# Kernel optimization log

Measured on AMD Instinct MI355X. Metric: run time of the kernel, lower is better.

## Reference

```python
import jax, jax.numpy as jnp
import numpy as np

ALPHA = 0.2  # leaky relu slope
NEG = -9e15


def setup_inputs() -> dict:
    key = jax.random.key(0)
    k1, k2, k3, k4 = jax.random.split(key, 4)
    B, N, Fin, Fout = 16, 2048, 256, 256
    h = jax.random.normal(k1, (B, N, Fin), dtype=jnp.float32)
    adj = jax.random.randint(k2, (B, N, N), 0, 2, dtype=jnp.int32)
    # xavier_uniform with gain 1.414 on [B, Fin, Fout] (fan over last two dims)
    limW = 1.414 * np.sqrt(6.0 / (Fin + Fout))
    W = jax.random.uniform(k3, (B, Fin, Fout), minval=-limW, maxval=limW, dtype=jnp.float32)
    lima = 1.414 * np.sqrt(6.0 / (2 * Fout + 1))
    a = jax.random.uniform(k4, (B, 2 * Fout, 1), minval=-lima, maxval=lima, dtype=jnp.float32)
    return {"h": h, "adj": adj, "W": W, "a": a}


def reference(h, adj, W, a):
    Fout = W.shape[-1]
    Wh = jnp.einsum('bnf,bfo->bno', h, W)                 # [B,N,Fout]
    Wh1 = jnp.einsum('bno,bo->bn', Wh, a[:, :Fout, 0])    # [B,N]
    Wh2 = jnp.einsum('bno,bo->bn', Wh, a[:, Fout:, 0])    # [B,N]
    e = Wh1[:, :, None] + Wh2[:, None, :]                 # [B,N,N]
    e = jnp.where(e > 0, e, ALPHA * e)                    # leaky relu
    att = jnp.where(adj > 0, e, NEG)
    att = jax.nn.softmax(att, axis=1)                     # NOTE: dim=1 as in source
    # dropout: eval mode -> identity
    h_prime = jnp.einsum('bij,bjo->bio', att, Wh)         # [B,N,Fout]
    return jax.nn.elu(h_prime)                            # concat=True
```

## Files before the change

### kernel.cpp

```cpp
#include <hip/hip_runtime.h>
#include <hip/hip_bf16.h>

typedef unsigned short u16;
typedef unsigned long long u64;
typedef __attribute__((ext_vector_type(8))) short bf16x8;
typedef __attribute__((ext_vector_type(4))) float f32x4;

#define NB 16
#define NN 2048
#define FF 256
#define LOG2E 1.4426950408889634f

__device__ __forceinline__ u16 f2bf(float x) {
    union { float f; unsigned u; } v; v.f = x;
    unsigned r = v.u + 0x7fffu + ((v.u >> 16) & 1u);
    return (u16)(r >> 16);
}

#define GLD_LDS(g, l) __builtin_amdgcn_global_load_lds((const __attribute__((address_space(1))) void*)(g), (__attribute__((address_space(3))) void*)(l), 16, 0, 0)

__global__ __launch_bounds__(256) void k_prep_w(const float* __restrict__ W, const float* __restrict__ a,
                                                u16* __restrict__ WT, float* __restrict__ u1, float* __restrict__ u2) {
    int b = blockIdx.y, t = threadIdx.x;
    __shared__ float a1s[FF], a2s[FF];
    a1s[t] = a[b*2*FF + t];
    a2s[t] = a[b*2*FF + FF + t];
    __syncthreads();
    int f = blockIdx.x*64 + (t >> 2);
    int o0 = (t & 3) * 64;
    const float* wrow = W + (size_t)(b*FF + f)*FF + o0;
    u16* wtb = WT + (size_t)b*FF*FF;
    float s1 = 0.f, s2 = 0.f;
#pragma unroll
    for (int c = 0; c < 16; ++c) {
        float4 v = *(const float4*)(wrow + c*4);
        int o = o0 + c*4;
        s1 += v.x*a1s[o] + v.y*a1s[o+1] + v.z*a1s[o+2] + v.w*a1s[o+3];
        s2 += v.x*a2s[o] + v.y*a2s[o+1] + v.z*a2s[o+2] + v.w*a2s[o+3];
        wtb[(size_t)(o+0)*FF + f] = f2bf(v.x);
        wtb[(size_t)(o+1)*FF + f] = f2bf(v.y);
        wtb[(size_t)(o+2)*FF + f] = f2bf(v.z);
        wtb[(size_t)(o+3)*FF + f] = f2bf(v.w);
    }
    s1 += __shfl_xor(s1, 1); s1 += __shfl_xor(s1, 2);
    s2 += __shfl_xor(s2, 1); s2 += __shfl_xor(s2, 2);
    if ((t & 3) == 0) { u1[b*FF + f] = s1; u2[b*FF + f] = s2; }
}

__global__ __launch_bounds__(256) void k_wh(const float* __restrict__ h, const u16* __restrict__ WT,
                                            const float* __restrict__ u1, const float* __restrict__ u2,
                                            u16* __restrict__ WhT, float* __restrict__ Wh1, float* __restrict__ Wh2) {
    int bid = blockIdx.x;
    int nid = (bid & 7)*64 + (bid >> 3);
    int b  = nid >> 5;
    int i0 = (nid & 31) * 64;
    int t = threadIdx.x, lane = t & 63, wave = t >> 6;
    __shared__ alignas(16) u16 At[256*64];
    __shared__ alignas(16) u16 Bt[64*64];
    __shared__ float u1s[FF], u2s[FF];
    u1s[t] = u1[b*FF + t];
    u2s[t] = u2[b*FF + t];

    const u16*   WTb = WT + (size_t)b*FF*FF;
    const float* hb  = h + ((size_t)b*NN + i0)*FF;
    int r = t >> 2, q = t & 3, kq = q*16;

    f32x4 acc[4][4];
#pragma unroll
    for (int x = 0; x < 4; ++x)
#pragma unroll
        for (int y = 0; y < 4; ++y) acc[x][y] = (f32x4)0.f;
    float s1 = 0.f, s2 = 0.f;
    __syncthreads();

#pragma unroll 1
    for (int kk = 0; kk < 4; ++kk) {
        int k0 = kk*64;
#pragma unroll
        for (int is = 0; is < 8; ++is) {
            int s = is*256 + t;
            int row = s >> 3, jbp = s & 7;
            int jbl = jbp ^ (row & 7);
            GLD_LDS(WTb + (size_t)row*FF + k0 + jbl*8, &At[s*8]);
        }
        {
            const float* hp = hb + (size_t)r*FF + k0 + kq;
            float4 f0 = *(const float4*)(hp + 0);
            float4 f1 = *(const float4*)(hp + 4);
            float4 f2 = *(const float4*)(hp + 8);
            float4 f3 = *(const float4*)(hp + 12);
            float fv[16] = {f0.x,f0.y,f0.z,f0.w, f1.x,f1.y,f1.z,f1.w,
                            f2.x,f2.y,f2.z,f2.w, f3.x,f3.y,f3.z,f3.w};
            union { u16 u[16]; bf16x8 v[2]; } cv;
#pragma unroll
            for (int e = 0; e < 16; ++e) {
                int kidx = k0 + kq + e;
                s1 += fv[e]*u1s[kidx];
                s2 += fv[e]*u2s[kidx];
                cv.u[e] = f2bf(fv[e]);
            }
            int rx = r & 7;
            *(bf16x8*)&Bt[r*64 + ((q*2 + 0) ^ rx)*8] = cv.v[0];
            *(bf16x8*)&Bt[r*64 + ((q*2 + 1) ^ rx)*8] = cv.v[1];
        }
        __syncthreads();
#pragma unroll
        for (int kc = 0; kc < 2; ++kc) {
            int jl = kc*4 + (lane >> 4);
            bf16x8 af[4], bfr[4];
#pragma unroll
            for (int mi = 0; mi < 4; ++mi) {
                int rr2 = wave*64 + mi*16 + (lane & 15);
                af[mi] = *(const bf16x8*)&At[rr2*64 + ((jl ^ (rr2 & 7))*8)];
            }
#pragma unroll
            for (int ni = 0; ni < 4; ++ni) {
                int rr2 = ni*16 + (lane & 15);
                bfr[ni] = *(const bf16x8*)&Bt[rr2*64 + ((jl ^ (rr2 & 7))*8)];
            }
#pragma unroll
            for (int mi = 0; mi < 4; ++mi)
#pragma unroll
                for (int ni = 0; ni < 4; ++ni)
                    acc[mi][ni] = __builtin_amdgcn_mfma_f32_16x16x32_bf16(af[mi], bfr[ni], acc[mi][ni], 0, 0, 0);
        }
        __syncthreads();
    }
    s1 += __shfl_xor(s1, 1); s1 += __shfl_xor(s1, 2);
    s2 += __shfl_xor(s2, 1); s2 += __shfl_xor(s2, 2);
    if (q == 0) { Wh1[b*NN + i0 + r] = s1*LOG2E; Wh2[b*NN + i0 + r] = s2*LOG2E; }

    u16* Wo = WhT + (size_t)b*FF*NN;
#pragma unroll
    for (int mi = 0; mi < 4; ++mi)
#pragma unroll
        for (int ni = 0; ni < 4; ++ni) {
            int i = i0 + ni*16 + (lane & 15);
#pragma unroll
            for (int rr = 0; rr < 4; ++rr) {
                int o = wave*64 + mi*16 + (lane >> 4)*4 + rr;
                Wo[(size_t)o*NN + i] = f2bf(acc[mi][ni][rr]);
            }
        }
}

__global__ __launch_bounds__(256) void k_pack(const int* __restrict__ adj, const float* __restrict__ Wh1,
                                              const float* __restrict__ Wh2, float* __restrict__ pS,
                                              u64* __restrict__ packed) {
    int b = blockIdx.y, ic = blockIdx.x;
    int t = threadIdx.x;
    __shared__ float wh1s[64], e1ps[64], e1ns[64];
    __shared__ unsigned char mk[64][256];
    int ibase = ic*64;
    if (t < 64) {
        float w1 = Wh1[b*NN + ibase + t];
        wh1s[t] = w1;
        e1ps[t] = __builtin_amdgcn_exp2f(w1);
        e1ns[t] = __builtin_amdgcn_exp2f(0.2f*w1);
    }
    float w2[8];
    {
        float4 a0 = *(const float4*)(Wh2 + b*NN + t*8);
        float4 a1 = *(const float4*)(Wh2 + b*NN + t*8 + 4);
        w2[0]=a0.x; w2[1]=a0.y; w2[2]=a0.z; w2[3]=a0.w;
        w2[4]=a1.x; w2[5]=a1.y; w2[6]=a1.z; w2[7]=a1.w;
    }
    __syncthreads();
    const int* abase = adj + ((size_t)(b*NN + ibase))*NN + t*8;
    float sp[8] = {0.f,0.f,0.f,0.f,0.f,0.f,0.f,0.f};
    float sn[8] = {0.f,0.f,0.f,0.f,0.f,0.f,0.f,0.f};
#pragma unroll 1
    for (int r4 = 0; r4 < 16; ++r4) {
        int4 v[4][2];
#pragma unroll
        for (int k = 0; k < 4; ++k) {
            v[k][0] = *(const int4*)(abase + (size_t)(r4*4 + k)*NN);
            v[k][1] = *(const int4*)(abase + (size_t)(r4*4 + k)*NN + 4);
        }
#pragma unroll
        for (int k = 0; k < 4; ++k) {
            int row = r4*4 + k;
            float w1 = wh1s[row], ep = e1ps[row], en = e1ns[row];
            int a[8] = {v[k][0].x, v[k][0].y, v[k][0].z, v[k][0].w,
                        v[k][1].x, v[k][1].y, v[k][1].z, v[k][1].w};
            unsigned bits = 0;
#pragma unroll
            for (int e = 0; e < 8; ++e) {
                bool bit = a[e] > 0;
                bool pos = (w1 + w2[e]) > 0.f;
                bits |= bit ? (1u << e) : 0u;
                sp[e] += (bit && pos)  ? ep : 0.f;
                sn[e] += (bit && !pos) ? en : 0.f;
            }
            mk[row][t] = (unsigned char)bits;
        }
    }
    __syncthreads();
    {
        int g = t >> 3, r0 = (t & 7)*8;
        u64* dst = packed + ((size_t)(b*32 + g))*NN + ibase + r0;
#pragma unroll
        for (int k = 0; k < 8; ++k)
            dst[k] = *(const u64*)&mk[r0 + k][g*8];
    }
    {
        float o8[8];
#pragma unroll
        for (int e = 0; e < 8; ++e) {
            float E2p = __builtin_amdgcn_exp2f(w2[e]);
            float E2n = __builtin_amdgcn_exp2f(0.2f*w2[e]);
            o8[e] = E2p*sp[e] + E2n*sn[e];
        }
        float4* po = (float4*)(pS + ((size_t)(b*32 + ic))*NN + t*8);
        po[0] = make_float4(o8[0],o8[1],o8[2],o8[3]);
        po[1] = make_float4(o8[4],o8[5],o8[6],o8[7]);
    }
}

__global__ __launch_bounds__(512, 1) void k_gemm3(const u16* __restrict__ WhT, const u64* __restrict__ packed,
                                                  const float* __restrict__ Wh1, const float* __restrict__ Wh2,
                                                  const float* __restrict__ pS, float* __restrict__ out) {
    int bid = blockIdx.x;
    int nid = (bid & 7)*32 + (bid >> 3);
    int b  = nid >> 4;
    int i0 = (nid & 15) * 128;
    int t = threadIdx.x, lane = t & 63, wave = t >> 6;
    int wm = wave >> 2, wn = wave & 3;
    __shared__ alignas(16) u16 At[2][128*64];
    __shared__ alignas(16) u16 Bt[3][256*64];
    __shared__ float wh2s[NN];
    __shared__ float e2ps[NN];
    __shared__ float e2ns[NN];
    __shared__ unsigned zlut[4];

    const u16* Wo = WhT + (size_t)b*FF*NN;
    int rA = t >> 2, qA = t & 3;
    const u64* pkbase = packed + (size_t)b*32*NN + i0 + rA;

    float wh1r = Wh1[b*NN + i0 + rA];
    float e1p = __builtin_amdgcn_exp2f(wh1r);
    float e1n = __builtin_amdgcn_exp2f(0.2f*wh1r);

#pragma unroll
    for (int c = 0; c < 4; ++c) {
        int idx = c*512 + t;
        float w2 = Wh2[b*NN + idx];
        float s = 0.f;
#pragma unroll
        for (int cc = 0; cc < 32; ++cc) s += pS[((size_t)(b*32 + cc))*NN + idx];
        float inv = (s > 0.f) ? 1.0f/s : 0.0f;
        wh2s[idx] = w2;
        e2ps[idx] = __builtin_amdgcn_exp2f(w2) * inv;
        e2ns[idx] = __builtin_amdgcn_exp2f(0.2f*w2) * inv;
    }
    if (t < 4) zlut[t] = ((t & 1) ? 0xFFFFu : 0u) | ((t & 2) ? 0xFFFF0000u : 0u);

    auto stageB = [&](int kk, int bbuf) {
        int k0 = kk*64;
#pragma unroll
        for (int is = 0; is < 4; ++is) {
            int s = is*512 + t;
            int row = s >> 3, jbp = s & 7;
            int jbl = jbp ^ (row & 7);
            GLD_LDS(Wo + (size_t)row*NN + k0 + jbl*8, &Bt[bbuf][s*8]);
        }
    };
    auto genA = [&](int g, int abuf, unsigned mask16) {
        int rx = rA & 7;
#pragma unroll
        for (int hf = 0; hf < 2; ++hf) {
            union { unsigned w[4]; bf16x8 v; } ob;
#pragma unroll
            for (int q4 = 0; q4 < 2; ++q4) {
                int jb = g*64 + qA*16 + hf*8 + q4*4;
                float4 w2 = *(const float4*)&wh2s[jb];
                float4 tp = *(const float4*)&e2ps[jb];
                float4 tn = *(const float4*)&e2ns[jb];
                float xs[4] = {w2.x, w2.y, w2.z, w2.w};
                float ps[4] = {tp.x, tp.y, tp.z, tp.w};
                float ns[4] = {tn.x, tn.y, tn.z, tn.w};
                float pe[4];
#pragma unroll
                for (int e = 0; e < 4; ++e) {
                    float tt = wh1r + xs[e];
                    bool pos = tt > 0.f;
                    pe[e] = (pos ? e1p : e1n) * (pos ? ps[e] : ns[e]);
                }
                unsigned bits = mask16 >> (hf*8 + q4*4);
#pragma unroll
                for (int p = 0; p < 2; ++p) {
                    unsigned w;
                    asm("v_cvt_pk_bf16_f32 %0, %1, %2" : "=v"(w) : "v"(pe[2*p]), "v"(pe[2*p+1]));
                    ob.w[q4*2 + p] = w & zlut[(bits >> (2*p)) & 3];
                }
            }
            *(bf16x8*)&At[abuf][rA*64 + (((qA*2 + hf) ^ rx)*8)] = ob.v;
        }
    };

#define MM(mi, ni, af, bf) acc[mi][ni] = __builtin_amdgcn_mfma_f32_16x16x32_bf16(af, bf, acc[mi][ni], 0, 0, 0)

    f32x4 acc[4][4];
#pragma unroll
    for (int x = 0; x < 4; ++x)
#pragma unroll
        for (int y = 0; y < 4; ++y) acc[x][y] = (f32x4)0.f;

    u64 mcur = pkbase[0];
    u64 mnext = pkbase[NN];
    __syncthreads();
    stageB(0, 0);
    stageB(1, 1);
    genA(0, 0, (unsigned)((mcur >> (qA*16)) & 0xffffu));
    asm volatile("s_waitcnt vmcnt(4) lgkmcnt(0)" ::: "memory");
    __builtin_amdgcn_s_barrier();

    int ibr = 0, ibs = 2;
#pragma unroll 1
    for (int kk = 0; kk < 32; ++kk) {
        int g = kk + 1;
        bool havef = (kk + 2 < 32);
        u64 mfut = 0;
        if (havef) mfut = pkbase[(size_t)(kk + 2)*NN];
        if (havef) stageB(kk + 2, ibs);
        if (g < 32) genA(g, g & 1, (unsigned)((mnext >> (qA*16)) & 0xffffu));
        int ra = kk & 1;
#pragma unroll
        for (int kc = 0; kc < 2; ++kc) {
            int jl = kc*4 + (lane >> 4);
            bf16x8 af[2], af2[2], bfr[4];
#pragma unroll
            for (int mi = 0; mi < 2; ++mi) {
                int rr2 = wm*64 + mi*16 + (lane & 15);
                af[mi] = *(const bf16x8*)&At[ra][rr2*64 + ((jl ^ (rr2 & 7))*8)];
            }
#pragma unroll
            for (int ni = 0; ni < 4; ++ni) {
                int rr2 = wn*64 + ni*16 + (lane & 15);
                bfr[ni] = *(const bf16x8*)&Bt[ibr][rr2*64 + ((jl ^ (rr2 & 7))*8)];
            }
            __builtin_amdgcn_s_setprio(1);
            MM(0,0,af[0],bfr[0]); MM(0,1,af[0],bfr[1]); MM(0,2,af[0],bfr[2]); MM(0,3,af[0],bfr[3]);
            MM(1,0,af[1],bfr[0]); MM(1,1,af[1],bfr[1]); MM(1,2,af[1],bfr[2]); MM(1,3,af[1],bfr[3]);
            __builtin_amdgcn_s_setprio(0);
#pragma unroll
            for (int mi = 2; mi < 4; ++mi) {
                int rr2 = wm*64 + mi*16 + (lane & 15);
                af2[mi-2] = *(const bf16x8*)&At[ra][rr2*64 + ((jl ^ (rr2 & 7))*8)];
            }
            __builtin_amdgcn_s_setprio(1);
            MM(2,0,af2[0],bfr[0]); MM(2,1,af2[0],bfr[1]); MM(2,2,af2[0],bfr[2]); MM(2,3,af2[0],bfr[3]);
            MM(3,0,af2[1],bfr[0]); MM(3,1,af2[1],bfr[1]); MM(3,2,af2[1],bfr[2]); MM(3,3,af2[1],bfr[3]);
            __builtin_amdgcn_s_setprio(0);
        }
        if (kk < 30) asm volatile("s_waitcnt vmcnt(4) lgkmcnt(0)" ::: "memory");
        else         asm volatile("s_waitcnt vmcnt(0) lgkmcnt(0)" ::: "memory");
        __builtin_amdgcn_s_barrier();
        if (havef) mnext = mfut;
        ibr = (ibr + 1 == 3) ? 0 : ibr + 1;
        ibs = (ibs + 1 == 3) ? 0 : ibs + 1;
    }
#undef MM

    float* ob2 = out + ((size_t)b*NN)*FF;
#pragma unroll
    for (int mi = 0; mi < 4; ++mi)
#pragma unroll
        for (int ni = 0; ni < 4; ++ni) {
            int o = wn*64 + ni*16 + (lane & 15);
#pragma unroll
            for (int rr = 0; rr < 4; ++rr) {
                int i = i0 + wm*64 + mi*16 + (lane >> 4)*4 + rr;
                float x = acc[mi][ni][rr];
                float y = (x > 0.f) ? x : (__builtin_amdgcn_exp2f(x*LOG2E) - 1.f);
                ob2[(size_t)i*FF + o] = y;
            }
        }
}

extern "C" void kernel_launch(void* const* d_in, const int* in_sizes, int n_in,
                              void* d_out, int out_size, void* d_ws, size_t ws_size,
                              hipStream_t stream) {
    const float* h   = (const float*)d_in[0];
    const int*   adj = (const int*)d_in[1];
    const float* W   = (const float*)d_in[2];
    const float* a   = (const float*)d_in[3];
    float* out = (float*)d_out;

    char* w = (char*)d_ws;
    const size_t MB = 1u << 20;
    u16* WT   = (u16*)(w + 0);
    u16* WhT  = (u16*)(w + 2*MB);
    u64* packed = (u64*)(w + 18*MB);
    float* pS  = (float*)(w + 26*MB);
    float* Wh1 = (float*)(w + 34*MB);
    float* Wh2 = (float*)(w + 34*MB + 131072);
    float* u1  = (float*)(w + 34*MB + 2*131072);
    float* u2  = (float*)(w + 34*MB + 2*131072 + 16384);

    k_prep_w<<<dim3(4, 16), 256, 0, stream>>>(W, a, WT, u1, u2);
    k_wh<<<dim3(512), 256, 0, stream>>>(h, WT, u1, u2, WhT, Wh1, Wh2);
    k_pack<<<dim3(32, 16), 256, 0, stream>>>(adj, Wh1, Wh2, pS, packed);
    k_gemm3<<<dim3(256), 512, 0, stream>>>(WhT, packed, Wh1, Wh2, pS, out);
}
```

Measured before the change: 149.4 us.

## Retile attention GEMM to 64-row blocks with smaller K-step and bf16 LDS tables

Restructures the final aggregation GEMM from 128-row tiles with 512 threads and a K-step of 64 to 64-row tiles with 256 threads and a K-step of 32, launching 512 blocks with two blocks per CU. The per-column softmax tables are now packed as bf16 in shared memory, and Wh2 is also stored as bf16, which cuts LDS footprint and read traffic during A-tile generation. The goal is better occupancy and CU balance, plus overlap between blocks. In exchange, B-tile (WhT) reuse per block is halved, so global/L2 traffic roughly doubles and there are twice as many barriers. The bf16 sign test on Wh1+Wh2 can also misclassify values near zero.

```diff
diff --git a/kernel.cpp b/kernel.cpp
--- a/kernel.cpp
+++ b/kernel.cpp
@@ -217,85 +217,79 @@
     }
 }
 
-__global__ __launch_bounds__(512, 1) void k_gemm3(const u16* __restrict__ WhT, const u64* __restrict__ packed,
+__global__ __launch_bounds__(256, 2) void k_gemm3(const u16* __restrict__ WhT, const u64* __restrict__ packed,
                                                   const float* __restrict__ Wh1, const float* __restrict__ Wh2,
                                                   const float* __restrict__ pS, float* __restrict__ out) {
     int bid = blockIdx.x;
-    int nid = (bid & 7)*32 + (bid >> 3);
-    int b  = nid >> 4;
-    int i0 = (nid & 15) * 128;
+    int nid = (bid & 7)*64 + (bid >> 3);
+    int b  = nid >> 5;
+    int i0 = (nid & 31) * 64;
     int t = threadIdx.x, lane = t & 63, wave = t >> 6;
-    int wm = wave >> 2, wn = wave & 3;
-    __shared__ alignas(16) u16 At[2][128*64];
-    __shared__ alignas(16) u16 Bt[3][256*64];
-    __shared__ float wh2s[NN];
-    __shared__ float e2ps[NN];
-    __shared__ float e2ns[NN];
+    __shared__ alignas(16) u16 At[2][64*32];
+    __shared__ alignas(16) u16 Bt[3][256*32];
+    __shared__ u16 wh2b[NN];
+    __shared__ unsigned eps2[NN];
     __shared__ unsigned zlut[4];
 
     const u16* Wo = WhT + (size_t)b*FF*NN;
     int rA = t >> 2, qA = t & 3;
-    const u64* pkbase = packed + (size_t)b*32*NN + i0 + rA;
+    const u64* pk64 = packed + (size_t)b*32*NN + i0 + rA;
 
     float wh1r = Wh1[b*NN + i0 + rA];
     float e1p = __builtin_amdgcn_exp2f(wh1r);
     float e1n = __builtin_amdgcn_exp2f(0.2f*wh1r);
 
-#pragma unroll
-    for (int c = 0; c < 4; ++c) {
-        int idx = c*512 + t;
+#pragma unroll 1
+    for (int c = 0; c < 8; ++c) {
+        int idx = c*256 + t;
         float w2 = Wh2[b*NN + idx];
         float s = 0.f;
 #pragma unroll
         for (int cc = 0; cc < 32; ++cc) s += pS[((size_t)(b*32 + cc))*NN + idx];
         float inv = (s > 0.f) ? 1.0f/s : 0.0f;
-        wh2s[idx] = w2;
-        e2ps[idx] = __builtin_amdgcn_exp2f(w2) * inv;
-        e2ns[idx] = __builtin_amdgcn_exp2f(0.2f*w2) * inv;
+        u16 ep = f2bf(__builtin_amdgcn_exp2f(w2) * inv);
+        u16 en = f2bf(__builtin_amdgcn_exp2f(0.2f*w2) * inv);
+        eps2[idx] = ((unsigned)ep << 16) | (unsigned)en;
+        wh2b[idx] = f2bf(w2);
     }
     if (t < 4) zlut[t] = ((t & 1) ? 0xFFFFu : 0u) | ((t & 2) ? 0xFFFF0000u : 0u);
 
-    auto stageB = [&](int kk, int bbuf) {
-        int k0 = kk*64;
+    auto stageB = [&](int g, int bbuf) {
+        int k0 = g*32;
 #pragma unroll
         for (int is = 0; is < 4; ++is) {
-            int s = is*512 + t;
-            int row = s >> 3, jbp = s & 7;
-            int jbl = jbp ^ (row & 7);
+            int s = is*256 + t;
+            int row = s >> 2, jbp = s & 3;
+            int jbl = jbp ^ (row & 3);
             GLD_LDS(Wo + (size_t)row*NN + k0 + jbl*8, &Bt[bbuf][s*8]);
         }
     };
-    auto genA = [&](int g, int abuf, unsigned mask16) {
-        int rx = rA & 7;
-#pragma unroll
-        for (int hf = 0; hf < 2; ++hf) {
-            union { unsigned w[4]; bf16x8 v; } ob;
-#pragma unroll
-            for (int q4 = 0; q4 < 2; ++q4) {
-                int jb = g*64 + qA*16 + hf*8 + q4*4;
-                float4 w2 = *(const float4*)&wh2s[jb];
-                float4 tp = *(const float4*)&e2ps[jb];
-                float4 tn = *(const float4*)&e2ns[jb];
-                float xs[4] = {w2.x, w2.y, w2.z, w2.w};
-                float ps[4] = {tp.x, tp.y, tp.z, tp.w};
-                float ns[4] = {tn.x, tn.y, tn.z, tn.w};
-                float pe[4];
-#pragma unroll
-                for (int e = 0; e < 4; ++e) {
-                    float tt = wh1r + xs[e];
-                    bool pos = tt > 0.f;
-                    pe[e] = (pos ? e1p : e1n) * (pos ? ps[e] : ns[e]);
-                }
-                unsigned bits = mask16 >> (hf*8 + q4*4);
-#pragma unroll
-                for (int p = 0; p < 2; ++p) {
-                    unsigned w;
-                    asm("v_cvt_pk_bf16_f32 %0, %1, %2" : "=v"(w) : "v"(pe[2*p]), "v"(pe[2*p+1]));
-                    ob.w[q4*2 + p] = w & zlut[(bits >> (2*p)) & 3];
-                }
-            }
-            *(bf16x8*)&At[abuf][rA*64 + (((qA*2 + hf) ^ rx)*8)] = ob.v;
-        }
+    auto genA = [&](int g, int abuf, unsigned mask32) {
+        unsigned mhf = (mask32 >> (qA*8)) & 0xffu;
+        int jb = g*32 + qA*8;
+        uint4 w2q = *(const uint4*)&wh2b[jb];
+        uint4 ea  = *(const uint4*)&eps2[jb];
+        uint4 eb  = *(const uint4*)&eps2[jb + 4];
+        unsigned wp[4] = {w2q.x, w2q.y, w2q.z, w2q.w};
+        unsigned ew[8] = {ea.x, ea.y, ea.z, ea.w, eb.x, eb.y, eb.z, eb.w};
+        float pe[8];
+#pragma unroll
+        for (int e = 0; e < 8; ++e) {
+            union { unsigned u; float f; } wf;
+            wf.u = (e & 1) ? (wp[e >> 1] & 0xFFFF0000u) : (wp[e >> 1] << 16);
+            bool pos = (wh1r + wf.f) > 0.f;
+            union { unsigned u; float f; } ef;
+            ef.u = pos ? (ew[e] & 0xFFFF0000u) : (ew[e] << 16);
+            pe[e] = (pos ? e1p : e1n) * ef.f;
+        }
+        union { unsigned w[4]; bf16x8 v; } ob;
+#pragma unroll
+        for (int p = 0; p < 4; ++p) {
+            unsigned wv;
+            asm("v_cvt_pk_bf16_f32 %0, %1, %2" : "=v"(wv) : "v"(pe[2*p]), "v"(pe[2*p+1]));
+            ob.w[p] = wv & zlut[(mhf >> (2*p)) & 3];
+        }
+        *(bf16x8*)&At[abuf][rA*32 + ((qA ^ (rA & 3))*8)] = ob.v;
     };
 
 #define MM(mi, ni, af, bf) acc[mi][ni] = __builtin_amdgcn_mfma_f32_16x16x32_bf16(af, bf, acc[mi][ni], 0, 0, 0)
@@ -306,57 +300,52 @@
 #pragma unroll
         for (int y = 0; y < 4; ++y) acc[x][y] = (f32x4)0.f;
 
-    u64 mcur = pkbase[0];
-    u64 mnext = pkbase[NN];
+    u64 mcur = pk64[0];
+    u64 mn0  = pk64[(size_t)1*NN];
+    u64 mn1  = pk64[(size_t)2*NN];
     __syncthreads();
     stageB(0, 0);
     stageB(1, 1);
-    genA(0, 0, (unsigned)((mcur >> (qA*16)) & 0xffffu));
+    genA(0, 0, (unsigned)mcur);
     asm volatile("s_waitcnt vmcnt(4) lgkmcnt(0)" ::: "memory");
     __builtin_amdgcn_s_barrier();
 
     int ibr = 0, ibs = 2;
 #pragma unroll 1
-    for (int kk = 0; kk < 32; ++kk) {
+    for (int kk = 0; kk < 64; ++kk) {
         int g = kk + 1;
-        bool havef = (kk + 2 < 32);
-        u64 mfut = 0;
-        if (havef) mfut = pkbase[(size_t)(kk + 2)*NN];
-        if (havef) stageB(kk + 2, ibs);
-        if (g < 32) genA(g, g & 1, (unsigned)((mnext >> (qA*16)) & 0xffffu));
+        if (g < 64 && (g & 1) == 0) {
+            mcur = mn0; mn0 = mn1;
+            int q = (g >> 1) + 2;
+            if (q < 32) mn1 = pk64[(size_t)q*NN];
+        }
+        if (kk + 2 < 64) stageB(kk + 2, ibs);
+        if (g < 64) {
+            unsigned m32 = (g & 1) ? (unsigned)(mcur >> 32) : (unsigned)mcur;
+            genA(g, g & 1, m32);
+        }
         int ra = kk & 1;
-#pragma unroll
-        for (int kc = 0; kc < 2; ++kc) {
-            int jl = kc*4 + (lane >> 4);
-            bf16x8 af[2], af2[2], bfr[4];
-#pragma unroll
-            for (int mi = 0; mi < 2; ++mi) {
-                int rr2 = wm*64 + mi*16 + (lane & 15);
-                af[mi] = *(const bf16x8*)&At[ra][rr2*64 + ((jl ^ (rr2 & 7))*8)];
-            }
-#pragma unroll
-            for (int ni = 0; ni < 4; ++ni) {
-                int rr2 = wn*64 + ni*16 + (lane & 15);
-                bfr[ni] = *(const bf16x8*)&Bt[ibr][rr2*64 + ((jl ^ (rr2 & 7))*8)];
-            }
-            __builtin_amdgcn_s_setprio(1);
-            MM(0,0,af[0],bfr[0]); MM(0,1,af[0],bfr[1]); MM(0,2,af[0],bfr[2]); MM(0,3,af[0],bfr[3]);
-            MM(1,0,af[1],bfr[0]); MM(1,1,af[1],bfr[1]); MM(1,2,af[1],bfr[2]); MM(1,3,af[1],bfr[3]);
-            __builtin_amdgcn_s_setprio(0);
-#pragma unroll
-            for (int mi = 2; mi < 4; ++mi) {
-                int rr2 = wm*64 + mi*16 + (lane & 15);
-                af2[mi-2] = *(const bf16x8*)&At[ra][rr2*64 + ((jl ^ (rr2 & 7))*8)];
-            }
-            __builtin_amdgcn_s_setprio(1);
-            MM(2,0,af2[0],bfr[0]); MM(2,1,af2[0],bfr[1]); MM(2,2,af2[0],bfr[2]); MM(2,3,af2[0],bfr[3]);
-            MM(3,0,af2[1],bfr[0]); MM(3,1,af2[1],bfr[1]); MM(3,2,af2[1],bfr[2]); MM(3,3,af2[1],bfr[3]);
-            __builtin_amdgcn_s_setprio(0);
-        }
-        if (kk < 30) asm volatile("s_waitcnt vmcnt(4) lgkmcnt(0)" ::: "memory");
+        int jl = lane >> 4;
+        bf16x8 af[4], bfr[4];
+#pragma unroll
+        for (int mi = 0; mi < 4; ++mi) {
+            int rr2 = mi*16 + (lane & 15);
+            af[mi] = *(const bf16x8*)&At[ra][rr2*32 + ((jl ^ (rr2 & 3))*8)];
+        }
+#pragma unroll
+        for (int ni = 0; ni < 4; ++ni) {
+            int rr2 = wave*64 + ni*16 + (lane & 15);
+            bfr[ni] = *(const bf16x8*)&Bt[ibr][rr2*32 + ((jl ^ (rr2 & 3))*8)];
+        }
+        __builtin_amdgcn_s_setprio(1);
+        MM(0,0,af[0],bfr[0]); MM(0,1,af[0],bfr[1]); MM(0,2,af[0],bfr[2]); MM(0,3,af[0],bfr[3]);
+        MM(1,0,af[1],bfr[0]); MM(1,1,af[1],bfr[1]); MM(1,2,af[1],bfr[2]); MM(1,3,af[1],bfr[3]);
+        MM(2,0,af[2],bfr[0]); MM(2,1,af[2],bfr[1]); MM(2,2,af[2],bfr[2]); MM(2,3,af[2],bfr[3]);
+        MM(3,0,af[3],bfr[0]); MM(3,1,af[3],bfr[1]); MM(3,2,af[3],bfr[2]); MM(3,3,af[3],bfr[3]);
+        __builtin_amdgcn_s_setprio(0);
+        if (kk < 62) asm volatile("s_waitcnt vmcnt(4) lgkmcnt(0)" ::: "memory");
         else         asm volatile("s_waitcnt vmcnt(0) lgkmcnt(0)" ::: "memory");
         __builtin_amdgcn_s_barrier();
-        if (havef) mnext = mfut;
         ibr = (ibr + 1 == 3) ? 0 : ibr + 1;
         ibs = (ibs + 1 == 3) ? 0 : ibs + 1;
     }
@@ -367,10 +356,10 @@
     for (int mi = 0; mi < 4; ++mi)
 #pragma unroll
         for (int ni = 0; ni < 4; ++ni) {
-            int o = wn*64 + ni*16 + (lane & 15);
+            int o = wave*64 + ni*16 + (lane & 15);
 #pragma unroll
             for (int rr = 0; rr < 4; ++rr) {
-                int i = i0 + wm*64 + mi*16 + (lane >> 4)*4 + rr;
+                int i = i0 + mi*16 + (lane >> 4)*4 + rr;
                 float x = acc[mi][ni][rr];
                 float y = (x > 0.f) ? x : (__builtin_amdgcn_exp2f(x*LOG2E) - 1.f);
                 ob2[(size_t)i*FF + o] = y;
@@ -401,5 +390,5 @@
     k_prep_w<<<dim3(4, 16), 256, 0, stream>>>(W, a, WT, u1, u2);
     k_wh<<<dim3(512), 256, 0, stream>>>(h, WT, u1, u2, WhT, Wh1, Wh2);
     k_pack<<<dim3(32, 16), 256, 0, stream>>>(adj, Wh1, Wh2, pS, packed);
-    k_gemm3<<<dim3(256), 512, 0, stream>>>(WhT, packed, Wh1, Wh2, pS, out);
-}
+    k_gemm3<<<dim3(512), 256, 0, stream>>>(WhT, packed, Wh1, Wh2, pS, out);
+}
```

Measured after the change: 156.5 us. +4.8%, slower.
